# Kernel tuning notes

Measured on AMD Instinct MI355X. Metric: run time of the kernel, lower is better.

The kernel has to match this reference:

```python
import jax, jax.numpy as jnp
import numpy as np
import math

N_NODES = 100000
N_EDGES = 3200000

_SQRT3 = math.sqrt(3.0)
_SQRT5 = math.sqrt(5.0)


def _spherical_harmonics_lmax2(v):
    """e3nn real spherical harmonics, lmax=2, normalize=True, normalization='component'.

    v: [E, 3] edge vectors (not necessarily unit).
    Returns [E, 9] = concat(Y0 [1], Y1 [3], Y2 [5]).
    """
    # normalize=True: evaluate SH on the unit vector
    u = v / jnp.linalg.norm(v, axis=1, keepdims=True)
    x, y, z = u[:, 0], u[:, 1], u[:, 2]
    # l=0 (component norm: *sqrt(1) = 1)
    sh0 = jnp.ones_like(x)
    # l=1 (component norm: *sqrt(3))
    sh1_0 = _SQRT3 * x
    sh1_1 = _SQRT3 * y
    sh1_2 = _SQRT3 * z
    # l=2 raw polynomials (norm-1 at unit vector), then *sqrt(5) for component norm
    x2, y2, z2 = x * x, y * y, z * z
    sh2_0 = _SQRT3 * x * z
    sh2_1 = _SQRT3 * x * y
    sh2_2 = y2 - 0.5 * (x2 + z2)
    sh2_3 = _SQRT3 * y * z
    sh2_4 = 0.5 * _SQRT3 * (z2 - x2)
    sh2 = _SQRT5 * jnp.stack([sh2_0, sh2_1, sh2_2, sh2_3, sh2_4], axis=-1)
    return jnp.concatenate(
        [sh0[:, None], jnp.stack([sh1_0, sh1_1, sh1_2], axis=-1), sh2], axis=-1
    )


def setup_inputs() -> dict:
    key = jax.random.key(0)
    k1, k2, k3 = jax.random.split(key, 3)
    pos = jax.random.normal(k1, (N_NODES, 3), dtype=jnp.float32)
    edge_index = jax.random.randint(k2, (2, N_EDGES), 0, N_NODES, dtype=jnp.int64)
    shift = jax.random.normal(k3, (N_EDGES, 3), dtype=jnp.float32)
    return {"pos": pos, "edge_index": edge_index, "shift": shift}


def reference(pos, edge_index, shift):
    # gather endpoints and form displacement vectors
    edge_vec = pos[edge_index[1]] - pos[edge_index[0]]  # [E, 3]
    edge_vec = edge_vec - shift
    edge_length = jnp.linalg.norm(edge_vec, axis=1)  # [E]
    edge_sh = _spherical_harmonics_lmax2(edge_vec)  # [E, 9]
    return (edge_vec, edge_length, edge_sh)
```

## Files before the change

kernel.cpp:

```cpp
#include <hip/hip_runtime.h>
#include <math.h>


#define SQRT3 1.7320508075688772f
#define SQRT5 2.2360679774997896f

typedef float v4f __attribute__((ext_vector_type(4)));

__global__ __launch_bounds__(256) void pack_pos4(
    const float* __restrict__ pos, float4* __restrict__ pos4, int n)
{
    int i = blockIdx.x * blockDim.x + threadIdx.x;
    if (i < n) {
        pos4[i] = make_float4(pos[3 * (size_t)i + 0],
                              pos[3 * (size_t)i + 1],
                              pos[3 * (size_t)i + 2], 0.0f);
    }
}

__global__ __launch_bounds__(256) void sh_edge_kernel(
    const float4* __restrict__ pos4,
    const float*  __restrict__ pos,
    const int*    __restrict__ edge_index,
    const float*  __restrict__ shift,
    float* __restrict__ out_vec,
    float* __restrict__ out_len,
    float* __restrict__ out_sh,
    int n_edges)
{
    __shared__ float s_shift[768];
    __shared__ float s_vec[768];
    __shared__ float s_len[256];
    __shared__ float s_sh[2304];

    const int tid  = threadIdx.x;
    const int base = blockIdx.x * 256;
    const int nblk = min(256, n_edges - base);
    const bool full = (nblk == 256);

    if (full) {
        const v4f* g = reinterpret_cast<const v4f*>(shift + 3 * (size_t)base);
        if (tid < 192) {
            v4f v = __builtin_nontemporal_load(&g[tid]);
            reinterpret_cast<v4f*>(s_shift)[tid] = v;
        }
    } else {
        for (int i = tid; i < 3 * nblk; i += 256)
            s_shift[i] = shift[3 * (size_t)base + i];
    }
    __syncthreads();

    if (tid < nblk) {
        const int e = base + tid;
        const int s = __builtin_nontemporal_load(&edge_index[e]);
        const int d = __builtin_nontemporal_load(&edge_index[n_edges + e]);

        float psx, psy, psz, pdx, pdy, pdz;
        if (pos4) {
            float4 ps = pos4[s];
            float4 pd = pos4[d];
            psx = ps.x; psy = ps.y; psz = ps.z;
            pdx = pd.x; pdy = pd.y; pdz = pd.z;
        } else {
            psx = pos[3 * (size_t)s + 0]; psy = pos[3 * (size_t)s + 1]; psz = pos[3 * (size_t)s + 2];
            pdx = pos[3 * (size_t)d + 0]; pdy = pos[3 * (size_t)d + 1]; pdz = pos[3 * (size_t)d + 2];
        }

        float x = pdx - psx - s_shift[3 * tid + 0];
        float y = pdy - psy - s_shift[3 * tid + 1];
        float z = pdz - psz - s_shift[3 * tid + 2];

        s_vec[3 * tid + 0] = x;
        s_vec[3 * tid + 1] = y;
        s_vec[3 * tid + 2] = z;

        float sq = x * x + y * y + z * z;
        float r  = rsqrtf(sq);
        s_len[tid] = sq * r;

        float nx = x * r, ny = y * r, nz = z * r;
        float x2 = nx * nx, y2 = ny * ny, z2 = nz * nz;

        float* o = s_sh + 9 * tid;
        o[0] = 1.0f;
        o[1] = SQRT3 * nx;
        o[2] = SQRT3 * ny;
        o[3] = SQRT3 * nz;
        o[4] = SQRT5 * SQRT3 * nx * nz;
        o[5] = SQRT5 * SQRT3 * nx * ny;
        o[6] = SQRT5 * (y2 - 0.5f * (x2 + z2));
        o[7] = SQRT5 * SQRT3 * ny * nz;
        o[8] = SQRT5 * 0.5f * SQRT3 * (z2 - x2);
    }
    __syncthreads();

    if (full) {
        v4f* gv = reinterpret_cast<v4f*>(out_vec + 3 * (size_t)base);
        const v4f* lv = reinterpret_cast<const v4f*>(s_vec);
        if (tid < 192) __builtin_nontemporal_store(lv[tid], &gv[tid]);

        v4f* gl = reinterpret_cast<v4f*>(out_len + (size_t)base);
        const v4f* ll = reinterpret_cast<const v4f*>(s_len);
        if (tid < 64) __builtin_nontemporal_store(ll[tid], &gl[tid]);

        v4f* gs = reinterpret_cast<v4f*>(out_sh + 9 * (size_t)base);
        const v4f* ls = reinterpret_cast<const v4f*>(s_sh);
        __builtin_nontemporal_store(ls[tid],       &gs[tid]);
        __builtin_nontemporal_store(ls[256 + tid], &gs[256 + tid]);
        if (tid < 64) __builtin_nontemporal_store(ls[512 + tid], &gs[512 + tid]);
    } else {
        for (int i = tid; i < 3 * nblk; i += 256) out_vec[3 * (size_t)base + i] = s_vec[i];
        for (int i = tid; i < nblk;     i += 256) out_len[(size_t)base + i]     = s_len[i];
        for (int i = tid; i < 9 * nblk; i += 256) out_sh[9 * (size_t)base + i]  = s_sh[i];
    }
}

extern "C" void kernel_launch(void* const* d_in, const int* in_sizes, int n_in,
                              void* d_out, int out_size, void* d_ws, size_t ws_size,
                              hipStream_t stream) {
    const float* pos        = (const float*)d_in[0];
    const int*   edge_index = (const int*)d_in[1];
    const float* shift      = (const float*)d_in[2];

    const int n_nodes = in_sizes[0] / 3;
    const int n_edges = in_sizes[2] / 3;

    float* out_vec = (float*)d_out;
    float* out_len = (float*)d_out + 3 * (size_t)n_edges;
    float* out_sh  = (float*)d_out + 4 * (size_t)n_edges;

    float4* pos4 = nullptr;
    if (ws_size >= (size_t)n_nodes * sizeof(float4)) {
        pos4 = (float4*)d_ws;
        int pblocks = (n_nodes + 255) / 256;
        pack_pos4<<<pblocks, 256, 0, stream>>>(pos, pos4, n_nodes);
    }

    const int blocks = (n_edges + 255) / 256;
    sh_edge_kernel<<<blocks, 256, 0, stream>>>(
        pos4, pos, edge_index, shift, out_vec, out_len, out_sh, n_edges);
}
```

Before: 235.3 us.

## Drop pos4 pack kernel, hoist gathers before shift staging, store length directly

Removes the separate pack_pos4 launch and gathers the three position floats straight from the original array. The index and position loads are moved ahead of the shift staging and barrier so their latency overlaps with the shared-memory fill. Edge length is now written directly per thread instead of being staged through shared memory. In exchange, each gathered position takes three scalar loads instead of one 16-byte load.

```diff
diff --git a/kernel.cpp b/kernel.cpp
--- a/kernel.cpp
+++ b/kernel.cpp
@@ -7,19 +7,7 @@
 
 typedef float v4f __attribute__((ext_vector_type(4)));
 
-__global__ __launch_bounds__(256) void pack_pos4(
-    const float* __restrict__ pos, float4* __restrict__ pos4, int n)
-{
-    int i = blockIdx.x * blockDim.x + threadIdx.x;
-    if (i < n) {
-        pos4[i] = make_float4(pos[3 * (size_t)i + 0],
-                              pos[3 * (size_t)i + 1],
-                              pos[3 * (size_t)i + 2], 0.0f);
-    }
-}
-
 __global__ __launch_bounds__(256) void sh_edge_kernel(
-    const float4* __restrict__ pos4,
     const float*  __restrict__ pos,
     const int*    __restrict__ edge_index,
     const float*  __restrict__ shift,
@@ -30,13 +18,23 @@
 {
     __shared__ float s_shift[768];
     __shared__ float s_vec[768];
-    __shared__ float s_len[256];
     __shared__ float s_sh[2304];
 
     const int tid  = threadIdx.x;
     const int base = blockIdx.x * 256;
     const int nblk = min(256, n_edges - base);
     const bool full = (nblk == 256);
+
+    float psx = 0.f, psy = 0.f, psz = 0.f, pdx = 0.f, pdy = 0.f, pdz = 0.f;
+    if (tid < nblk) {
+        const int e = base + tid;
+        const int s = __builtin_nontemporal_load(&edge_index[e]);
+        const int d = __builtin_nontemporal_load(&edge_index[n_edges + e]);
+        const float* ps = pos + 3 * (size_t)s;
+        const float* pd = pos + 3 * (size_t)d;
+        psx = ps[0]; psy = ps[1]; psz = ps[2];
+        pdx = pd[0]; pdy = pd[1]; pdz = pd[2];
+    }
 
     if (full) {
         const v4f* g = reinterpret_cast<const v4f*>(shift + 3 * (size_t)base);
@@ -52,19 +50,6 @@
 
     if (tid < nblk) {
         const int e = base + tid;
-        const int s = __builtin_nontemporal_load(&edge_index[e]);
-        const int d = __builtin_nontemporal_load(&edge_index[n_edges + e]);
-
-        float psx, psy, psz, pdx, pdy, pdz;
-        if (pos4) {
-            float4 ps = pos4[s];
-            float4 pd = pos4[d];
-            psx = ps.x; psy = ps.y; psz = ps.z;
-            pdx = pd.x; pdy = pd.y; pdz = pd.z;
-        } else {
-            psx = pos[3 * (size_t)s + 0]; psy = pos[3 * (size_t)s + 1]; psz = pos[3 * (size_t)s + 2];
-            pdx = pos[3 * (size_t)d + 0]; pdy = pos[3 * (size_t)d + 1]; pdz = pos[3 * (size_t)d + 2];
-        }
 
         float x = pdx - psx - s_shift[3 * tid + 0];
         float y = pdy - psy - s_shift[3 * tid + 1];
@@ -76,7 +61,7 @@
 
         float sq = x * x + y * y + z * z;
         float r  = rsqrtf(sq);
-        s_len[tid] = sq * r;
+        __builtin_nontemporal_store(sq * r, &out_len[e]);
 
         float nx = x * r, ny = y * r, nz = z * r;
         float x2 = nx * nx, y2 = ny * ny, z2 = nz * nz;
@@ -99,10 +84,6 @@
         const v4f* lv = reinterpret_cast<const v4f*>(s_vec);
         if (tid < 192) __builtin_nontemporal_store(lv[tid], &gv[tid]);
 
-        v4f* gl = reinterpret_cast<v4f*>(out_len + (size_t)base);
-        const v4f* ll = reinterpret_cast<const v4f*>(s_len);
-        if (tid < 64) __builtin_nontemporal_store(ll[tid], &gl[tid]);
-
         v4f* gs = reinterpret_cast<v4f*>(out_sh + 9 * (size_t)base);
         const v4f* ls = reinterpret_cast<const v4f*>(s_sh);
         __builtin_nontemporal_store(ls[tid],       &gs[tid]);
@@ -110,7 +91,6 @@
         if (tid < 64) __builtin_nontemporal_store(ls[512 + tid], &gs[512 + tid]);
     } else {
         for (int i = tid; i < 3 * nblk; i += 256) out_vec[3 * (size_t)base + i] = s_vec[i];
-        for (int i = tid; i < nblk;     i += 256) out_len[(size_t)base + i]     = s_len[i];
         for (int i = tid; i < 9 * nblk; i += 256) out_sh[9 * (size_t)base + i]  = s_sh[i];
     }
 }
@@ -122,21 +102,13 @@
     const int*   edge_index = (const int*)d_in[1];
     const float* shift      = (const float*)d_in[2];
 
-    const int n_nodes = in_sizes[0] / 3;
     const int n_edges = in_sizes[2] / 3;
 
     float* out_vec = (float*)d_out;
     float* out_len = (float*)d_out + 3 * (size_t)n_edges;
     float* out_sh  = (float*)d_out + 4 * (size_t)n_edges;
 
-    float4* pos4 = nullptr;
-    if (ws_size >= (size_t)n_nodes * sizeof(float4)) {
-        pos4 = (float4*)d_ws;
-        int pblocks = (n_nodes + 255) / 256;
-        pack_pos4<<<pblocks, 256, 0, stream>>>(pos, pos4, n_nodes);
-    }
-
     const int blocks = (n_edges + 255) / 256;
     sh_edge_kernel<<<blocks, 256, 0, stream>>>(
-        pos4, pos, edge_index, shift, out_vec, out_len, out_sh, n_edges);
+        pos, edge_index, shift, out_vec, out_len, out_sh, n_edges);
 }
```

After: 246.8 us. 1.05x slower.
